# Performance work log

Hardware: AMD Instinct MI355X
Metric: run time of the kernel (lower is better)

Reference implementation:

```python
import jax, jax.numpy as jnp
import numpy as np

DELTA = 0.5
WEIGHT = 1.0
W = 1.85 + DELTA  # ego width  (+ safety delta)
H = 4.084 + DELTA  # ego length (+ safety delta)

F = 6          # planning futures
N = 1000000    # gt boxes per future (padded)


def setup_inputs() -> dict:
    key = jax.random.key(0)
    k1, k2, k3 = jax.random.split(key, 3)
    return {
        "sdc_traj_all": jax.random.normal(k1, (1, F, 2), dtype=jnp.float32),
        "sdc_planning_gt": jax.random.normal(k2, (1, F, 3), dtype=jnp.float32),
        "sdc_planning_gt_mask": jnp.ones((1, F, 2), dtype=jnp.float32),
        "future_gt_corners": jax.random.normal(k3, (F, N, 4, 2), dtype=jnp.float32),
        "box_mask": jnp.ones((F, N), dtype=bool),
    }


def _sdc_corners(x, y, theta):
    # local box corners [4,2] (w/2, l/2 pattern as in to_corners)
    local = jnp.array([[W / 2, -H / 2], [W / 2, H / 2],
                       [-W / 2, H / 2], [-W / 2, -H / 2]], dtype=x.dtype)  # [4,2]
    c, s = jnp.cos(theta), jnp.sin(theta)  # [F]
    # rot_mat = [[c, s], [-s, c]]; new_corners = (rot @ local.T + t).T
    rot = jnp.stack([jnp.stack([c, s], -1), jnp.stack([-s, c], -1)], -2)  # [F,2,2]
    corners = jnp.einsum('fij,kj->fki', rot, local)  # [F,4,2]
    return corners + jnp.stack([x, y], -1)[:, None, :]  # [F,4,2]


def reference(sdc_traj_all, sdc_planning_gt, sdc_planning_gt_mask, future_gt_corners, box_mask):
    x = sdc_traj_all[0, :, 0]
    y = sdc_traj_all[0, :, 1]
    theta = sdc_planning_gt[0, :, 2].astype(sdc_traj_all.dtype)
    sdc = _sdc_corners(x, y, theta)  # [F,4,2]

    # ego AABB per future
    xa1 = sdc[..., 0].max(-1)[:, None]  # [F,1]
    ya1 = sdc[..., 1].max(-1)[:, None]
    xa2 = sdc[..., 0].min(-1)[:, None]
    ya2 = sdc[..., 1].min(-1)[:, None]

    # gt boxes AABB per (future, box)
    xb1 = future_gt_corners[..., 0].max(-1)  # [F,N]
    yb1 = future_gt_corners[..., 1].max(-1)
    xb2 = future_gt_corners[..., 0].min(-1)
    yb2 = future_gt_corners[..., 1].min(-1)

    w = jnp.clip(jnp.minimum(xa1, xb1) - jnp.maximum(xa2, xb2), 0)
    h = jnp.clip(jnp.minimum(ya1, yb1) - jnp.maximum(ya2, yb2), 0)
    inter = jnp.where(box_mask, w * h, 0.0)
    return (inter.sum() * WEIGHT).reshape(1)
```

## Files before the change

kernel.cpp:

```cpp
#include <hip/hip_runtime.h>
#include <math.h>

#define NFRAMES 6
#define NBOX    1000000
#define TOTAL   (NFRAMES * NBOX)

#define BPT     4
#define NTHREADS (TOTAL / BPT)
#define BLOCK   256
#define NBLOCKS ((NTHREADS + BLOCK - 1) / BLOCK)

#define HALF_W  (2.35f * 0.5f)
#define HALF_H  (4.584f * 0.5f)

__global__ __launch_bounds__(BLOCK) void CollisionLoss_55327768708655_kernel(
    const float* __restrict__ traj,
    const float* __restrict__ gt,
    const float* __restrict__ corners,
    const int*   __restrict__ mask,
    float* __restrict__ partials)
{
    __shared__ float4 s_frame[NFRAMES];
    if (threadIdx.x < NFRAMES) {
        int f = threadIdx.x;
        float x  = traj[f * 2 + 0];
        float y  = traj[f * 2 + 1];
        float th = gt[f * 3 + 2];
        float c = cosf(th), s = sinf(th);
        float ex = fabsf(c) * HALF_W + fabsf(s) * HALF_H;
        float ey = fabsf(s) * HALF_W + fabsf(c) * HALF_H;
        s_frame[f] = make_float4(x + ex, y + ey, x - ex, y - ey);
    }
    __syncthreads();

    float acc = 0.0f;
    int tid = blockIdx.x * BLOCK + threadIdx.x;
    if (tid < NTHREADS) {
        const float4* p = (const float4*)corners + (size_t)tid * (2 * BPT);
        float4 A[8];
        #pragma unroll
        for (int j = 0; j < 8; ++j) A[j] = p[j];
        int4 m = ((const int4*)mask)[tid];

        int f = (tid * BPT) / NBOX;
        float4 fr = s_frame[f];

        int M[4] = {m.x, m.y, m.z, m.w};
        #pragma unroll
        for (int j = 0; j < BPT; ++j) {
            float4 a = A[2 * j + 0];
            float4 b = A[2 * j + 1];
            float xb1 = fmaxf(fmaxf(a.x, a.z), fmaxf(b.x, b.z));
            float xb2 = fminf(fminf(a.x, a.z), fminf(b.x, b.z));
            float yb1 = fmaxf(fmaxf(a.y, a.w), fmaxf(b.y, b.w));
            float yb2 = fminf(fminf(a.y, a.w), fminf(b.y, b.w));
            float w = fminf(fr.x, xb1) - fmaxf(fr.z, xb2);
            float h = fminf(fr.y, yb1) - fmaxf(fr.w, yb2);
            float v = fmaxf(w, 0.0f) * fmaxf(h, 0.0f);
            acc += M[j] ? v : 0.0f;
        }
    }

    #pragma unroll
    for (int off = 32; off > 0; off >>= 1)
        acc += __shfl_down(acc, off, 64);

    __shared__ float s_part[BLOCK / 64];
    int lane = threadIdx.x & 63;
    int wave = threadIdx.x >> 6;
    if (lane == 0) s_part[wave] = acc;
    __syncthreads();
    if (threadIdx.x == 0)
        partials[blockIdx.x] = s_part[0] + s_part[1] + s_part[2] + s_part[3];
}

__global__ __launch_bounds__(BLOCK) void finalize_kernel(
    const float* __restrict__ partials, float* __restrict__ out)
{
    float acc = 0.0f;
    for (int i = threadIdx.x; i < NBLOCKS; i += BLOCK)
        acc += partials[i];
    #pragma unroll
    for (int off = 32; off > 0; off >>= 1)
        acc += __shfl_down(acc, off, 64);
    __shared__ float s_part[BLOCK / 64];
    int lane = threadIdx.x & 63;
    int wave = threadIdx.x >> 6;
    if (lane == 0) s_part[wave] = acc;
    __syncthreads();
    if (threadIdx.x == 0)
        out[0] = s_part[0] + s_part[1] + s_part[2] + s_part[3];
}

extern "C" void kernel_launch(void* const* d_in, const int* in_sizes, int n_in,
                              void* d_out, int out_size, void* d_ws, size_t ws_size,
                              hipStream_t stream) {
    const float* traj     = (const float*)d_in[0];
    const float* gt       = (const float*)d_in[1];
    const float* corners  = (const float*)d_in[3];
    const int*   mask     = (const int*)d_in[4];
    float* partials       = (float*)d_ws;
    float* out            = (float*)d_out;

    CollisionLoss_55327768708655_kernel<<<NBLOCKS, BLOCK, 0, stream>>>(
        traj, gt, corners, mask, partials);
    finalize_kernel<<<1, BLOCK, 0, stream>>>(partials, out);
}
```

Baseline: 288.3 us.

## Use coalesced per-lane float4 loads with DPP pair reduction and grid-stride waves

Each lane now loads one float4 (half a box) per step, so a wave's loads are contiguous and fully coalesced instead of each thread reading 128 contiguous bytes. Adjacent lanes combine their half-box min/max through a DPP quad-perm swap, and each lane adds half the intersection so the pair sums to the full value. The grid becomes a fixed 2048 blocks with a wave-level grid-stride loop over 128-box chunks, which cuts the number of partials and the launch size. The mask is now read as a scalar per box, duplicated across lane pairs, instead of as an int4 load.

```diff
diff --git a/kernel.cpp b/kernel.cpp
--- a/kernel.cpp
+++ b/kernel.cpp
@@ -3,15 +3,22 @@
 
 #define NFRAMES 6
 #define NBOX    1000000
-#define TOTAL   (NFRAMES * NBOX)
-
-#define BPT     4
-#define NTHREADS (TOTAL / BPT)
-#define BLOCK   256
-#define NBLOCKS ((NTHREADS + BLOCK - 1) / BLOCK)
+#define TOTALBOX (NFRAMES * NBOX)
+#define TOTALF4  (2 * TOTALBOX)
+#define CHUNK_F4 256
+#define CHUNK_BOX 128
+#define NCHUNKS  (TOTALF4 / CHUNK_F4)
+#define BLOCK    256
+#define NBLOCKS  2048
+#define NWAVES   (NBLOCKS * (BLOCK / 64))
 
 #define HALF_W  (2.35f * 0.5f)
 #define HALF_H  (4.584f * 0.5f)
+
+__device__ __forceinline__ float dpp_swap_pair(float x) {
+    return __int_as_float(__builtin_amdgcn_update_dpp(
+        0, __float_as_int(x), 0xB1, 0xF, 0xF, true));
+}
 
 __global__ __launch_bounds__(BLOCK) void CollisionLoss_55327768708655_kernel(
     const float* __restrict__ traj,
@@ -33,42 +40,41 @@
     }
     __syncthreads();
 
+    const float4* __restrict__ cp = (const float4*)corners;
+    const int lane = threadIdx.x & 63;
+    const int k    = lane >> 1;
+    const int wid  = blockIdx.x * (BLOCK / 64) + (threadIdx.x >> 6);
+
     float acc = 0.0f;
-    int tid = blockIdx.x * BLOCK + threadIdx.x;
-    if (tid < NTHREADS) {
-        const float4* p = (const float4*)corners + (size_t)tid * (2 * BPT);
-        float4 A[8];
+    for (int chunk = wid; chunk < NCHUNKS; chunk += NWAVES) {
+        const float4* base = cp + (size_t)chunk * CHUNK_F4 + lane;
+        const int basebox  = chunk * CHUNK_BOX;
         #pragma unroll
-        for (int j = 0; j < 8; ++j) A[j] = p[j];
-        int4 m = ((const int4*)mask)[tid];
+        for (int j = 0; j < 4; ++j) {
+            float4 v = base[j * 64];
+            float pxmax = fmaxf(v.x, v.z), pxmin = fminf(v.x, v.z);
+            float pymax = fmaxf(v.y, v.w), pymin = fminf(v.y, v.w);
+            float xb1 = fmaxf(pxmax, dpp_swap_pair(pxmax));
+            float xb2 = fminf(pxmin, dpp_swap_pair(pxmin));
+            float yb1 = fmaxf(pymax, dpp_swap_pair(pymax));
+            float yb2 = fminf(pymin, dpp_swap_pair(pymin));
 
-        int f = (tid * BPT) / NBOX;
-        float4 fr = s_frame[f];
+            int b = basebox + j * 32 + k;
+            int f = (int)((unsigned)b / (unsigned)NBOX);
+            float4 fr = s_frame[f];
 
-        int M[4] = {m.x, m.y, m.z, m.w};
-        #pragma unroll
-        for (int j = 0; j < BPT; ++j) {
-            float4 a = A[2 * j + 0];
-            float4 b = A[2 * j + 1];
-            float xb1 = fmaxf(fmaxf(a.x, a.z), fmaxf(b.x, b.z));
-            float xb2 = fminf(fminf(a.x, a.z), fminf(b.x, b.z));
-            float yb1 = fmaxf(fmaxf(a.y, a.w), fmaxf(b.y, b.w));
-            float yb2 = fminf(fminf(a.y, a.w), fminf(b.y, b.w));
             float w = fminf(fr.x, xb1) - fmaxf(fr.z, xb2);
             float h = fminf(fr.y, yb1) - fmaxf(fr.w, yb2);
-            float v = fmaxf(w, 0.0f) * fmaxf(h, 0.0f);
-            acc += M[j] ? v : 0.0f;
+            float a = fmaxf(w, 0.0f) * fmaxf(h, 0.0f);
+            acc += mask[b] ? 0.5f * a : 0.0f;
         }
     }
 
     #pragma unroll
     for (int off = 32; off > 0; off >>= 1)
         acc += __shfl_down(acc, off, 64);
-
     __shared__ float s_part[BLOCK / 64];
-    int lane = threadIdx.x & 63;
-    int wave = threadIdx.x >> 6;
-    if (lane == 0) s_part[wave] = acc;
+    if (lane == 0) s_part[threadIdx.x >> 6] = acc;
     __syncthreads();
     if (threadIdx.x == 0)
         partials[blockIdx.x] = s_part[0] + s_part[1] + s_part[2] + s_part[3];
```

Result: no change. 287.4 us (-0.3%).
